# Optimization experiments

Hardware: AMD Instinct MI355X
Metric: run time of the kernel (lower is better)

## Reference

```python
import jax, jax.numpy as jnp
import numpy as np
from jax import lax

BN_EPS = 1e-3  # keras BatchNormalization default epsilon
TOP_K = 2      # keep_top_k


def _conv3(x, k, b, s):
    # x: NDHWC, k: DHWIO, 'SAME' padding like keras Conv3D(padding='same')
    y = lax.conv_general_dilated(x, k, (s, s, s), 'SAME',
                                 dimension_numbers=('NDHWC', 'DHWIO', 'NDHWC'))
    return y + b


def _bn(x, g, be, m, v):
    # inference-mode batch norm with moving statistics
    return g * (x - m) * lax.rsqrt(v + BN_EPS) + be


def setup_inputs() -> dict:
    key = jax.random.key(0)
    ks = jax.random.split(key, 64)
    B, S = 16, 96
    nf, ksz, nE, nb = 32, 3, 8, 4
    inp = {"x": jax.random.normal(ks[0], (B, S, S, S, 1), jnp.float32)}
    cin = 1
    for i in range(nb):
        cout = nf * 2 ** i
        base = 1 + 6 * i
        inp["k%d" % i] = jax.random.normal(ks[base], (ksz, ksz, ksz, cin, cout), jnp.float32) * 0.05
        inp["b%d" % i] = jnp.zeros((cout,), jnp.float32)
        inp["g%d" % i] = 1.0 + 0.1 * jax.random.normal(ks[base + 1], (cout,), jnp.float32)
        inp["be%d" % i] = 0.1 * jax.random.normal(ks[base + 2], (cout,), jnp.float32)
        inp["m%d" % i] = 0.1 * jax.random.normal(ks[base + 3], (cout,), jnp.float32)
        inp["v%d" % i] = jax.random.uniform(ks[base + 4], (cout,), jnp.float32, 0.5, 1.5)
        cin = cout
    c = nf * 2 ** (nb - 1)  # 256
    inp["w1k"] = jax.random.normal(ks[30], (1, 1, 1, c, c), jnp.float32) * 0.05
    inp["w1b"] = jnp.zeros((c,), jnp.float32)
    inp["wg"] = 1.0 + 0.1 * jax.random.normal(ks[31], (c,), jnp.float32)
    inp["wbe"] = 0.1 * jax.random.normal(ks[32], (c,), jnp.float32)
    inp["wm"] = 0.1 * jax.random.normal(ks[33], (c,), jnp.float32)
    inp["wv"] = jax.random.uniform(ks[34], (c,), jnp.float32, 0.5, 1.5)
    inp["w2k"] = jax.random.normal(ks[35], (1, 1, 1, c, nE), jnp.float32) * 0.05
    inp["w2b"] = jnp.zeros((nE,), jnp.float32)
    return inp


def reference(x, k0, b0, g0, be0, m0, v0, k1, b1, g1, be1, m1, v1,
              k2, b2, g2, be2, m2, v2, k3, b3, g3, be3, m3, v3,
              w1k, w1b, wg, wbe, wm, wv, w2k, w2b):
    blocks = [(k0, b0, g0, be0, m0, v0), (k1, b1, g1, be1, m1, v1),
              (k2, b2, g2, be2, m2, v2), (k3, b3, g3, be3, m3, v3)]
    h = x
    for k, b, g, be, m, v in blocks:  # EncoderBlock: Conv3D(stride 2)+BN+ReLU
        h = jax.nn.relu(_bn(_conv3(h, k, b, 2), g, be, m, v))
    h = jnp.mean(h, axis=(1, 2, 3), keepdims=True)  # GAP, [B,1,1,1,256]
    w = _conv3(h, w1k, w1b, 1)
    w = jax.nn.relu(_bn(w, wg, wbe, wm, wv))
    w = _conv3(w, w2k, w2b, 1)  # [B,1,1,1,n_experts]
    # noisy-top-k gating (noise disabled at inference): mask non-top-k to -inf
    top_vals = lax.top_k(w, TOP_K)[0]
    thr = top_vals[..., TOP_K - 1:TOP_K]
    w = jnp.where(w >= thr, w, -jnp.inf)
    return jax.nn.softmax(w, axis=-1)
```

## Files before the change

kernel.cpp:

```cpp
#include <hip/hip_runtime.h>
#include <math.h>

#define BN_EPS 1e-3f

typedef __attribute__((ext_vector_type(8))) unsigned short ushort8v;
typedef __attribute__((ext_vector_type(8))) short short8v;
typedef __attribute__((ext_vector_type(4))) float f32x4;
typedef __attribute__((ext_vector_type(4))) unsigned int uint4v;

__device__ __forceinline__ float4 f4load(const float* p) {
    return *reinterpret_cast<const float4*>(p);
}
__device__ __forceinline__ float bf2f(unsigned short u) {
    union { unsigned int i; float f; } w; w.i = ((unsigned int)u) << 16; return w.f;
}
__device__ __forceinline__ unsigned short f2bf(float f) {
    union { float fv; unsigned int i; } w; w.fv = f;
    unsigned int lsb = (w.i >> 16) & 1u;
    w.i += 0x7fffu + lsb;
    return (unsigned short)(w.i >> 16);
}
__device__ __forceinline__ unsigned cvtpk(float lo, float hi) {
    unsigned r;
    asm("v_cvt_pk_bf16_f32 %0, %1, %2" : "=v"(r) : "v"(lo), "v"(hi));
    return r;
}
__device__ __forceinline__ void st_pair(unsigned short* p0, unsigned short* p1,
                                        float f0, float f1) {
    unsigned u = cvtpk(f0, f1);
    p0[0] = (unsigned short)u;
    p1[0] = (unsigned short)(u >> 16);
}
template<int N> __device__ __forceinline__ void waitv() {
    asm volatile("s_waitcnt vmcnt(%0)" :: "n"(N) : "memory");
}

#define GLOAD_LDS16(g, l)                                                     \
    __builtin_amdgcn_global_load_lds(                                         \
        (const __attribute__((address_space(1))) void*)(const void*)(g),      \
        (__attribute__((address_space(3))) void*)(void*)(l), 16, 0, 0)
#define GLOAD_LDS4(g, l)                                                      \
    __builtin_amdgcn_global_load_lds(                                         \
        (const __attribute__((address_space(1))) void*)(const void*)(g),      \
        (__attribute__((address_space(3))) void*)(void*)(l), 4, 0, 0)

template<int CIN, int COUT>
__device__ __forceinline__ void wprep_body(
    const float* __restrict__ k, unsigned short* __restrict__ wt, int blk)
{
    constexpr int NS = COUT / 16;
    constexpr int KS = CIN / 32;
    int idx = blk * 256 + (int)threadIdx.x;
    if (idx >= 27 * KS * NS * 64) return;
    int lane = idx & 63;
    int nsg  = (idx >> 6) % NS;
    int it   = idx / (64 * NS);
    int tap  = it / KS;
    int ks   = it - tap * KS;
    int sg = lane >> 4, lr = lane & 15;
    int cout = nsg * 16 + lr;
    ushort8v o;
    #pragma unroll
    for (int j = 0; j < 8; ++j) {
        int ci = ks * 32 + sg * 8 + j;
        o[j] = f2bf(k[(size_t)(tap * CIN + ci) * COUT + cout]);
    }
    *reinterpret_cast<ushort8v*>(wt + (size_t)idx * 8) = o;
}

__global__ __launch_bounds__(256) void wprep_all(
    const float* __restrict__ k0,
    const float* __restrict__ k1, const float* __restrict__ k2, const float* __restrict__ k3,
    unsigned short* __restrict__ w0f,
    unsigned short* __restrict__ w1, unsigned short* __restrict__ w2, unsigned short* __restrict__ w3,
    unsigned short* __restrict__ zp)
{
    int b = blockIdx.x;
    if (b < 27)       wprep_body<32, 64>(k1, w1, b);
    else if (b < 135) wprep_body<64, 128>(k2, w2, b - 27);
    else if (b < 567) wprep_body<128, 256>(k3, w3, b - 135);
    else {
        reinterpret_cast<unsigned int*>(zp)[threadIdx.x] = 0u;
        if (threadIdx.x < 128) {
            int ns = threadIdx.x >> 6, lane = threadIdx.x & 63;
            int sg = lane >> 4, lr = lane & 15;
            ushort8v o;
            #pragma unroll
            for (int j = 0; j < 8; ++j) {
                int t = sg * 8 + j;
                o[j] = (t < 27) ? f2bf(k0[t * 32 + ns * 16 + lr]) : (unsigned short)0;
            }
            *reinterpret_cast<ushort8v*>(w0f + (ns * 64 + lane) * 8) = o;
        }
    }
}

__global__ __launch_bounds__(256) void conv0_lds(
    const float* __restrict__ x, const unsigned short* __restrict__ w0f,
    const float* __restrict__ zf,
    const float* __restrict__ b, const float* __restrict__ g,
    const float* __restrict__ be, const float* __restrict__ m,
    const float* __restrict__ v, unsigned short* __restrict__ y)
{
    __shared__ __attribute__((aligned(16))) float tile[81 * 32];
    __shared__ float side[84];
    __shared__ float zslot;

    const int l   = threadIdx.x & 63;
    const int wid = threadIdx.x >> 6;
    const int sg  = l >> 4;
    const int lr  = l & 15;

    int bb = blockIdx.x;
    const int owt = bb % 3;  bb /= 3;
    const int oht = bb % 12; bb /= 12;
    const int odt = bb % 12; const int n = bb / 12;

    const int id0 = odt * 8, ih0 = oht * 8, iw0 = owt * 32;

    if (threadIdx.x == 0) zslot = 0.f;

    #pragma unroll
    for (int q0 = 0; q0 < 648; q0 += 256) {
        int qq = q0 + wid * 64;
        int q = qq + l;
        if (qq < 648 && q < 648) {
            int row = q >> 3, c = q & 7;
            int dd = row / 9, hh = row - dd * 9;
            int id = id0 + dd, ih = ih0 + hh;
            const float* src = (id < 96 && ih < 96)
                ? x + ((size_t)(n * 96 + id) * 96 + ih) * 96 + iw0 + c * 4
                : zf;
            GLOAD_LDS16(src, (char*)tile + (size_t)qq * 16);
        }
    }
    {
        int row = (wid == 0) ? l : ((wid == 1 && l < 17) ? 64 + l : -1);
        if (row >= 0) {
            int dd = row / 9, hh = row - dd * 9;
            int id = id0 + dd, ih = ih0 + hh;
            const float* src = (id < 96 && ih < 96 && iw0 + 32 < 96)
                ? x + ((size_t)(n * 96 + id) * 96 + ih) * 96 + iw0 + 32
                : zf;
            GLOAD_LDS4(src, (char*)side + (wid == 0 ? 0 : 256));
        }
    }
    __syncthreads();

    const short8v B0 = *(const short8v*)(w0f + l * 8);
    const short8v B1 = *(const short8v*)(w0f + (64 + l) * 8);

    int ej[8], wwj[8];
    bool validj[8], sidej[8];
    #pragma unroll
    for (int j = 0; j < 8; ++j) {
        int tap = sg * 8 + j;
        int t = (tap < 27) ? tap : 0;
        int kd = t / 9, r9 = t - kd * 9, kh = r9 / 3, kw = r9 - kh * 3;
        ej[j] = kd * 9 + kh;
        wwj[j] = 2 * lr + kw;
        sidej[j] = (wwj[j] >= 32);
        validj[j] = (tap < 27);
    }

    f32x4 acc[4][2];
    #pragma unroll
    for (int mi = 0; mi < 4; ++mi) {
        acc[mi][0] = (f32x4){0.f, 0.f, 0.f, 0.f};
        acc[mi][1] = (f32x4){0.f, 0.f, 0.f, 0.f};
    }

    #pragma unroll
    for (int mi = 0; mi < 4; ++mi) {
        float av[8];
        #pragma unroll
        for (int j = 0; j < 8; ++j) {
            int row = 18 * wid + 2 * mi + ej[j];
            const float* p = sidej[j] ? &side[row] : &tile[row * 32 + wwj[j]];
            p = validj[j] ? p : &zslot;
            av[j] = *p;
        }
        uint4v au;
        au[0] = cvtpk(av[0], av[1]);
        au[1] = cvtpk(av[2], av[3]);
        au[2] = cvtpk(av[4], av[5]);
        au[3] = cvtpk(av[6], av[7]);
        short8v a = __builtin_bit_cast(short8v, au);
        acc[mi][0] = __builtin_amdgcn_mfma_f32_16x16x32_bf16(a, B0, acc[mi][0], 0, 0, 0);
        acc[mi][1] = __builtin_amdgcn_mfma_f32_16x16x32_bf16(a, B1, acc[mi][1], 0, 0, 0);
    }

    float S[2], T[2];
    #pragma unroll
    for (int ns = 0; ns < 2; ++ns) {
        int c = ns * 16 + lr;
        float sc = g[c] * rsqrtf(v[c] + BN_EPS);
        S[ns] = sc;
        T[ns] = (b[c] - m[c]) * sc + be[c];
    }
    const int odG = odt * 4 + wid;
    #pragma unroll
    for (int mi = 0; mi < 4; ++mi) {
        int oh = oht * 4 + mi;
        unsigned short* yrow =
            y + (((size_t)(n * 48 + odG) * 48 + oh) * 48 + owt * 16) * 32;
        #pragma unroll
        for (int i = 0; i < 4; i += 2) {
            unsigned short* yp0 = yrow + (size_t)(sg * 4 + i) * 32;
            unsigned short* yp1 = yp0 + 32;
            st_pair(yp0 + lr, yp1 + lr,
                    fmaxf(acc[mi][0][i]     * S[0] + T[0], 0.f),
                    fmaxf(acc[mi][0][i + 1] * S[0] + T[0], 0.f));
            st_pair(yp0 + 16 + lr, yp1 + 16 + lr,
                    fmaxf(acc[mi][1][i]     * S[1] + T[1], 0.f),
                    fmaxf(acc[mi][1][i + 1] * S[1] + T[1], 0.f));
        }
    }
}

template<int CIN, int COUT, int INS, int OUTS, int MW, int NSW, int NH,
         int CSPLIT, int KU>
__global__ __launch_bounds__(256, 2) void conv_mfma_lds(
    const unsigned short* __restrict__ x, const unsigned short* __restrict__ wt,
    const unsigned short* __restrict__ zp,
    const float* __restrict__ b, const float* __restrict__ g,
    const float* __restrict__ be, const float* __restrict__ m,
    const float* __restrict__ v, unsigned short* __restrict__ y)
{
    constexpr int NSfull = COUT / 16;
    constexpr int NSB = NSW * NH;
    constexpr int KS = CIN / 32;
    constexpr int NITK = 27 * KS;
    constexpr int NIT = NITK / KU;
    constexpr int MGROUPS = 4 / NH;
    constexpr int MTILE = MGROUPS * MW * 16;
    constexpr int BSTEP = NSB * KU * 1024;
    constexpr int ASTEP = MGROUPS * MW * KU * 1024;
    constexpr int STRIDE = BSTEP + ASTEP;
    constexpr int BL = (NSB * KU) / 4;
    constexpr int AL = MW * KU;
    static_assert(NSB * CSPLIT == NSfull && NITK % KU == 0 && (NSB * KU) % 4 == 0, "tiling");
    static_assert(NIT >= 3, "pipeline depth");

    __shared__ __attribute__((aligned(16))) char lds[3 * STRIDE];

    const int l   = threadIdx.x & 63;
    const int wid = threadIdx.x >> 6;
    const int sg  = l >> 4;
    const int lr  = l & 15;

    const int mblk   = blockIdx.x / CSPLIT;
    const int cchunk = blockIdx.x % CSPLIT;
    const int mgroup = wid / NH;
    const int ngroup = wid % NH;
    const int gCoutBase = (cchunk * NSB + ngroup * NSW) * 16;
    const int vwave = mblk * MTILE + mgroup * MW * 16;

    const unsigned short* ap0[MW];
    unsigned smask[MW];
    #pragma unroll
    for (int mi = 0; mi < MW; ++mi) {
        int vA = vwave + mi * 16 + lr;
        int owA = vA % OUTS; int t1 = vA / OUTS;
        int ohA = t1 % OUTS; int t2 = t1 / OUTS;
        int odA = t2 % OUTS; int nA = t2 / OUTS;
        ap0[mi] = x + ((((size_t)nA * INS + 2 * odA) * INS + 2 * ohA) * INS + 2 * owA) * CIN + sg * 8;
        smask[mi] = ((odA == OUTS - 1) ? 0x07FC0000u : 0u)
                  | ((ohA == OUTS - 1) ? 0x070381C0u : 0u)
                  | ((owA == OUTS - 1) ? 0x04924924u : 0u);
    }

    const unsigned short* zpl = (const unsigned short*)((const char*)zp + l * 16);

    f32x4 acc[MW][NSW];
    #pragma unroll
    for (int mi = 0; mi < MW; ++mi)
        #pragma unroll
        for (int ns = 0; ns < NSW; ++ns) acc[mi][ns] = (f32x4){0.f, 0.f, 0.f, 0.f};

    auto stage = [&](int ito, int p) {
        char* dst = &lds[p * STRIDE];
        #pragma unroll
        for (int c = 0; c < BL; ++c) {
            int idx  = c * 256 + (int)threadIdx.x;
            int lane = idx & 63;
            int sub  = idx >> 6;
            int u    = sub / NSB;
            int grp  = sub % NSB;
            int it   = ito * KU + u;
            const unsigned short* src =
                wt + ((size_t)(it * NSfull + cchunk * NSB + grp) * 64 + lane) * 8;
            GLOAD_LDS16(src, dst + sub * 1024);
        }
        if (ngroup == 0) {
            #pragma unroll
            for (int u = 0; u < KU; ++u) {
                int it = ito * KU + u;
                int tap = (KS == 1) ? it : it / KS;
                int ks  = (KS == 1) ? 0  : it - tap * KS;
                int kd = tap / 9, r9 = tap - kd * 9, kh = r9 / 3, kw = r9 - kh * 3;
                size_t aoff = (size_t)((kd * INS + kh) * INS + kw) * CIN + ks * 32;
                #pragma unroll
                for (int mi = 0; mi < MW; ++mi) {
                    const unsigned short* ga =
                        ((smask[mi] >> tap) & 1u) ? zpl : (ap0[mi] + aoff);
                    GLOAD_LDS16(ga, dst + BSTEP + ((mgroup * MW + mi) * KU + u) * 1024);
                }
            }
        }
    };

    auto computestep = [&](const char* buf) {
        #pragma unroll
        for (int u = 0; u < KU; ++u) {
            short8v Bf[NSW], Af[MW];
            #pragma unroll
            for (int ns = 0; ns < NSW; ++ns)
                Bf[ns] = *(const short8v*)(buf + (u * NSB + ngroup * NSW + ns) * 1024 + l * 16);
            #pragma unroll
            for (int mi = 0; mi < MW; ++mi)
                Af[mi] = *(const short8v*)(buf + BSTEP + ((mgroup * MW + mi) * KU + u) * 1024 + l * 16);
            #pragma unroll
            for (int mi = 0; mi < MW; ++mi)
                #pragma unroll
                for (int ns = 0; ns < NSW; ++ns)
                    acc[mi][ns] = __builtin_amdgcn_mfma_f32_16x16x32_bf16(Af[mi], Bf[ns], acc[mi][ns], 0, 0, 0);
        }
    };

    stage(0, 0);
    stage(1, 1);
    #pragma unroll 1
    for (int ito = 0; ito < NIT - 1; ++ito) {
        if (ngroup == 0) waitv<BL + AL>(); else waitv<BL>();
        __builtin_amdgcn_s_barrier();
        asm volatile("" ::: "memory");
        if (ito + 2 < NIT) stage(ito + 2, (ito + 2) % 3);
        computestep(&lds[(ito % 3) * STRIDE]);
    }
    waitv<0>();
    __builtin_amdgcn_s_barrier();
    asm volatile("" ::: "memory");
    computestep(&lds[((NIT - 1) % 3) * STRIDE]);

    float S[NSW], T[NSW];
    #pragma unroll
    for (int ns = 0; ns < NSW; ++ns) {
        int c = gCoutBase + ns * 16 + lr;
        float sc = g[c] * rsqrtf(v[c] + BN_EPS);
        S[ns] = sc;
        T[ns] = (b[c] - m[c]) * sc + be[c];
    }
    #pragma unroll
    for (int mi = 0; mi < MW; ++mi) {
        #pragma unroll
        for (int i = 0; i < 4; i += 2) {
            int vD0 = vwave + mi * 16 + sg * 4 + i;
            int vD1 = vD0 + 1;
            int ow0 = vD0 % OUTS; int u1 = vD0 / OUTS;
            int oh0 = u1 % OUTS; int u2 = u1 / OUTS;
            int od0 = u2 % OUTS; int n0 = u2 / OUTS;
            unsigned short* yp0 =
                y + ((((size_t)n0 * OUTS + od0) * OUTS + oh0) * OUTS + ow0) * COUT + gCoutBase + lr;
            int ow1 = vD1 % OUTS; int w1 = vD1 / OUTS;
            int oh1 = w1 % OUTS; int w2 = w1 / OUTS;
            int od1 = w2 % OUTS; int n1 = w2 / OUTS;
            unsigned short* yp1 =
                y + ((((size_t)n1 * OUTS + od1) * OUTS + oh1) * OUTS + ow1) * COUT + gCoutBase + lr;
            #pragma unroll
            for (int ns = 0; ns < NSW; ++ns)
                st_pair(yp0 + ns * 16, yp1 + ns * 16,
                        fmaxf(acc[mi][ns][i]     * S[ns] + T[ns], 0.f),
                        fmaxf(acc[mi][ns][i + 1] * S[ns] + T[ns], 0.f));
        }
    }
}

__global__ __launch_bounds__(256) void head_kernel(
    const unsigned short* __restrict__ x4,
    const float* __restrict__ w1k, const float* __restrict__ w1b,
    const float* __restrict__ wg,  const float* __restrict__ wbe,
    const float* __restrict__ wm,  const float* __restrict__ wv,
    const float* __restrict__ w2k, const float* __restrict__ w2b,
    float* __restrict__ out)
{
    __shared__ float part[8][256];
    __shared__ float h[256];
    __shared__ float r[256];
    __shared__ float logits[8];

    const int n = blockIdx.x;
    const int t = threadIdx.x;
    const int c8 = t & 31;
    const int pg = t >> 5;

    const unsigned short* xb = x4 + (size_t)n * 216 * 256 + c8 * 8;
    float s[8] = {0.f, 0.f, 0.f, 0.f, 0.f, 0.f, 0.f, 0.f};
    for (int i = pg; i < 216; i += 8) {
        ushort8v v8 = *reinterpret_cast<const ushort8v*>(xb + (size_t)i * 256);
        #pragma unroll
        for (int j = 0; j < 8; ++j) s[j] += bf2f(v8[j]);
    }
    #pragma unroll
    for (int j = 0; j < 8; ++j) part[pg][c8 * 8 + j] = s[j];
    __syncthreads();

    float a = 0.f;
    #pragma unroll
    for (int gi = 0; gi < 8; ++gi) a += part[gi][t];
    h[t] = a * (1.0f / 216.0f);
    __syncthreads();

    float acc = w1b[t];
    #pragma unroll 4
    for (int ci = 0; ci < 256; ++ci) acc += h[ci] * w1k[ci * 256 + t];
    float sc = wg[t] * rsqrtf(wv[t] + BN_EPS);
    acc = (acc - wm[t]) * sc + wbe[t];
    r[t] = fmaxf(acc, 0.f);
    __syncthreads();

    if (t < 8) {
        float a2 = w2b[t];
        for (int ci = 0; ci < 256; ++ci) a2 += r[ci] * w2k[ci * 8 + t];
        logits[t] = a2;
    }
    __syncthreads();

    if (t == 0) {
        float m1 = -INFINITY, m2 = -INFINITY;
        for (int e = 0; e < 8; ++e) {
            float val = logits[e];
            if (val > m1) { m2 = m1; m1 = val; }
            else if (val > m2) { m2 = val; }
        }
        float thr = m2;
        float ex[8]; float sum = 0.f;
        for (int e = 0; e < 8; ++e) {
            float val = (logits[e] >= thr) ? logits[e] : -INFINITY;
            ex[e] = expf(val - m1);
            sum += ex[e];
        }
        float inv = 1.0f / sum;
        for (int e = 0; e < 8; ++e) out[n * 8 + e] = ex[e] * inv;
    }
}

extern "C" void kernel_launch(void* const* d_in, const int* in_sizes, int n_in,
                              void* d_out, int out_size, void* d_ws, size_t ws_size,
                              hipStream_t stream) {
    const float* x   = (const float*)d_in[0];
    const float* k0  = (const float*)d_in[1];
    const float* b0  = (const float*)d_in[2];
    const float* g0  = (const float*)d_in[3];
    const float* be0 = (const float*)d_in[4];
    const float* m0  = (const float*)d_in[5];
    const float* v0  = (const float*)d_in[6];
    const float* k1  = (const float*)d_in[7];
    const float* b1  = (const float*)d_in[8];
    const float* g1  = (const float*)d_in[9];
    const float* be1 = (const float*)d_in[10];
    const float* m1  = (const float*)d_in[11];
    const float* v1  = (const float*)d_in[12];
    const float* k2  = (const float*)d_in[13];
    const float* b2  = (const float*)d_in[14];
    const float* g2  = (const float*)d_in[15];
    const float* be2 = (const float*)d_in[16];
    const float* m2  = (const float*)d_in[17];
    const float* v2  = (const float*)d_in[18];
    const float* k3  = (const float*)d_in[19];
    const float* b3  = (const float*)d_in[20];
    const float* g3  = (const float*)d_in[21];
    const float* be3 = (const float*)d_in[22];
    const float* m3  = (const float*)d_in[23];
    const float* v3  = (const float*)d_in[24];
    const float* w1k = (const float*)d_in[25];
    const float* w1b = (const float*)d_in[26];
    const float* wg  = (const float*)d_in[27];
    const float* wbe = (const float*)d_in[28];
    const float* wm  = (const float*)d_in[29];
    const float* wv  = (const float*)d_in[30];
    const float* w2k = (const float*)d_in[31];
    const float* w2b = (const float*)d_in[32];

    unsigned short* x1  = (unsigned short*)d_ws;
    unsigned short* x2  = x1 + 56623104;
    unsigned short* x3  = x2 + 14155776;
    unsigned short* x4  = x3 + 3538944;
    unsigned short* Wt1 = x4 + 884736;
    unsigned short* Wt2 = Wt1 + 55296;
    unsigned short* Wt3 = Wt2 + 221184;
    unsigned short* zp  = Wt3 + 884736;
    unsigned short* W0f = zp + 512;

    wprep_all<<<568, 256, 0, stream>>>(k0, k1, k2, k3, W0f, Wt1, Wt2, Wt3, zp);
    conv0_lds<<<6912, 256, 0, stream>>>(x, W0f, (const float*)zp, b0, g0, be0, m0, v0, x1);
    conv_mfma_lds<32, 64, 48, 24, 2, 4, 1, 1, 1><<<1728, 256, 0, stream>>>(x1, Wt1, zp, b1, g1, be1, m1, v1, x2);
    conv_mfma_lds<64, 128, 24, 12, 1, 4, 2, 1, 1><<<864, 256, 0, stream>>>(x2, Wt2, zp, b2, g2, be2, m2, v2, x3);
    conv_mfma_lds<128, 256, 12, 6, 1, 1, 4, 4, 2><<<864, 256, 0, stream>>>(x3, Wt3, zp, b3, g3, be3, m3, v3, x4);
    head_kernel<<<16, 256, 0, stream>>>(x4, w1k, w1b, wg, wbe, wm, wv, w2k, w2b, (float*)d_out);
}
```

Baseline: 195.8 us.

## Restructure conv0 tap layout with padded LDS tile and register-cached rows

```diff
diff --git a/kernel.cpp b/kernel.cpp
--- a/kernel.cpp
+++ b/kernel.cpp
@@ -39,10 +39,6 @@
     __builtin_amdgcn_global_load_lds(                                         \
         (const __attribute__((address_space(1))) void*)(const void*)(g),      \
         (__attribute__((address_space(3))) void*)(void*)(l), 16, 0, 0)
-#define GLOAD_LDS4(g, l)                                                      \
-    __builtin_amdgcn_global_load_lds(                                         \
-        (const __attribute__((address_space(1))) void*)(const void*)(g),      \
-        (__attribute__((address_space(3))) void*)(void*)(l), 4, 0, 0)
 
 template<int CIN, int COUT>
 __device__ __forceinline__ void wprep_body(
@@ -81,16 +77,21 @@
     else if (b < 567) wprep_body<128, 256>(k3, w3, b - 135);
     else {
         reinterpret_cast<unsigned int*>(zp)[threadIdx.x] = 0u;
-        if (threadIdx.x < 128) {
-            int ns = threadIdx.x >> 6, lane = threadIdx.x & 63;
+        {
+            int t = (int)threadIdx.x;
+            int lane = t & 63;
+            int mf = (t >> 6) & 1;
+            int ns = t >> 7;
             int sg = lane >> 4, lr = lane & 15;
             ushort8v o;
             #pragma unroll
             for (int j = 0; j < 8; ++j) {
-                int t = sg * 8 + j;
-                o[j] = (t < 27) ? f2bf(k0[t * 32 + ns * 16 + lr]) : (unsigned short)0;
+                int jj = mf * 8 + j;
+                bool valid = (sg < 3) && (jj < 9);
+                int tap = sg * 9 + jj;
+                o[j] = valid ? f2bf(k0[tap * 32 + ns * 16 + lr]) : (unsigned short)0;
             }
-            *reinterpret_cast<ushort8v*>(w0f + (ns * 64 + lane) * 8) = o;
+            *reinterpret_cast<ushort8v*>(w0f + (size_t)t * 8) = o;
         }
     }
 }
@@ -102,9 +103,7 @@
     const float* __restrict__ be, const float* __restrict__ m,
     const float* __restrict__ v, unsigned short* __restrict__ y)
 {
-    __shared__ __attribute__((aligned(16))) float tile[81 * 32];
-    __shared__ float side[84];
-    __shared__ float zslot;
+    __shared__ __attribute__((aligned(16))) float tile[81 * 36];
 
     const int l   = threadIdx.x & 63;
     const int wid = threadIdx.x >> 6;
@@ -118,49 +117,38 @@
 
     const int id0 = odt * 8, ih0 = oht * 8, iw0 = owt * 32;
 
-    if (threadIdx.x == 0) zslot = 0.f;
-
-    #pragma unroll
-    for (int q0 = 0; q0 < 648; q0 += 256) {
+    #pragma unroll
+    for (int q0 = 0; q0 < 729; q0 += 256) {
         int qq = q0 + wid * 64;
-        int q = qq + l;
-        if (qq < 648 && q < 648) {
-            int row = q >> 3, c = q & 7;
+        int q  = qq + l;
+        if (qq < 729 && q < 729) {
+            int row = q / 9, c = q - row * 9;
             int dd = row / 9, hh = row - dd * 9;
             int id = id0 + dd, ih = ih0 + hh;
-            const float* src = (id < 96 && ih < 96)
+            const float* src =
+                (id < 96 && ih < 96 && (c < 8 || iw0 + 32 < 96))
                 ? x + ((size_t)(n * 96 + id) * 96 + ih) * 96 + iw0 + c * 4
                 : zf;
             GLOAD_LDS16(src, (char*)tile + (size_t)qq * 16);
         }
     }
+    __syncthreads();
+
+    const short8v B00 = *(const short8v*)(w0f + (size_t)(0 * 64 + l) * 8);
+    const short8v B01 = *(const short8v*)(w0f + (size_t)(1 * 64 + l) * 8);
+    const short8v B10 = *(const short8v*)(w0f + (size_t)(2 * 64 + l) * 8);
+    const short8v B11 = *(const short8v*)(w0f + (size_t)(3 * 64 + l) * 8);
+
+    float rc[9][3];
     {
-        int row = (wid == 0) ? l : ((wid == 1 && l < 17) ? 64 + l : -1);
-        if (row >= 0) {
-            int dd = row / 9, hh = row - dd * 9;
-            int id = id0 + dd, ih = ih0 + hh;
-            const float* src = (id < 96 && ih < 96 && iw0 + 32 < 96)
-                ? x + ((size_t)(n * 96 + id) * 96 + ih) * 96 + iw0 + 32
-                : zf;
-            GLOAD_LDS4(src, (char*)side + (wid == 0 ? 0 : 256));
-        }
-    }
-    __syncthreads();
-
-    const short8v B0 = *(const short8v*)(w0f + l * 8);
-    const short8v B1 = *(const short8v*)(w0f + (64 + l) * 8);
-
-    int ej[8], wwj[8];
-    bool validj[8], sidej[8];
-    #pragma unroll
-    for (int j = 0; j < 8; ++j) {
-        int tap = sg * 8 + j;
-        int t = (tap < 27) ? tap : 0;
-        int kd = t / 9, r9 = t - kd * 9, kh = r9 / 3, kw = r9 - kh * 3;
-        ej[j] = kd * 9 + kh;
-        wwj[j] = 2 * lr + kw;
-        sidej[j] = (wwj[j] >= 32);
-        validj[j] = (tap < 27);
+        int dcl = (sg < 3) ? (2 * wid + sg) : 0;
+        const float* rb = tile + (size_t)(dcl * 9) * 36 + 2 * lr;
+        #pragma unroll
+        for (int r = 0; r < 9; ++r) {
+            float2 lo = *reinterpret_cast<const float2*>(rb + r * 36);
+            rc[r][0] = lo.x; rc[r][1] = lo.y;
+            rc[r][2] = rb[r * 36 + 2];
+        }
     }
 
     f32x4 acc[4][2];
@@ -172,22 +160,21 @@
 
     #pragma unroll
     for (int mi = 0; mi < 4; ++mi) {
-        float av[8];
-        #pragma unroll
-        for (int j = 0; j < 8; ++j) {
-            int row = 18 * wid + 2 * mi + ej[j];
-            const float* p = sidej[j] ? &side[row] : &tile[row * 32 + wwj[j]];
-            p = validj[j] ? p : &zslot;
-            av[j] = *p;
-        }
-        uint4v au;
-        au[0] = cvtpk(av[0], av[1]);
-        au[1] = cvtpk(av[2], av[3]);
-        au[2] = cvtpk(av[4], av[5]);
-        au[3] = cvtpk(av[6], av[7]);
-        short8v a = __builtin_bit_cast(short8v, au);
-        acc[mi][0] = __builtin_amdgcn_mfma_f32_16x16x32_bf16(a, B0, acc[mi][0], 0, 0, 0);
-        acc[mi][1] = __builtin_amdgcn_mfma_f32_16x16x32_bf16(a, B1, acc[mi][1], 0, 0, 0);
+        const int h0 = 2 * mi;
+        uint4v au0;
+        au0[0] = cvtpk(rc[h0][0],     rc[h0][1]);
+        au0[1] = cvtpk(rc[h0][2],     rc[h0 + 1][0]);
+        au0[2] = cvtpk(rc[h0 + 1][1], rc[h0 + 1][2]);
+        au0[3] = cvtpk(rc[h0 + 2][0], rc[h0 + 2][1]);
+        short8v a0 = __builtin_bit_cast(short8v, au0);
+        uint4v au1;
+        au1[0] = cvtpk(rc[h0 + 2][2], 0.f);
+        au1[1] = 0; au1[2] = 0; au1[3] = 0;
+        short8v a1 = __builtin_bit_cast(short8v, au1);
+        acc[mi][0] = __builtin_amdgcn_mfma_f32_16x16x32_bf16(a0, B00, acc[mi][0], 0, 0, 0);
+        acc[mi][0] = __builtin_amdgcn_mfma_f32_16x16x32_bf16(a1, B01, acc[mi][0], 0, 0, 0);
+        acc[mi][1] = __builtin_amdgcn_mfma_f32_16x16x32_bf16(a0, B10, acc[mi][1], 0, 0, 0);
+        acc[mi][1] = __builtin_amdgcn_mfma_f32_16x16x32_bf16(a1, B11, acc[mi][1], 0, 0, 0);
     }
 
     float S[2], T[2];
@@ -494,7 +481,7 @@
 
     wprep_all<<<568, 256, 0, stream>>>(k0, k1, k2, k3, W0f, Wt1, Wt2, Wt3, zp);
     conv0_lds<<<6912, 256, 0, stream>>>(x, W0f, (const float*)zp, b0, g0, be0, m0, v0, x1);
-    conv_mfma_lds<32, 64, 48, 24, 2, 4, 1, 1, 1><<<1728, 256, 0, stream>>>(x1, Wt1, zp, b1, g1, be1, m1, v1, x2);
+    conv_mfma_lds<32, 64, 48, 24, 3, 4, 1, 1, 1><<<1152, 256, 0, stream>>>(x1, Wt1, zp, b1, g1, be1, m1, v1, x2);
     conv_mfma_lds<64, 128, 24, 12, 1, 4, 2, 1, 1><<<864, 256, 0, stream>>>(x2, Wt2, zp, b2, g2, be2, m2, v2, x3);
     conv_mfma_lds<128, 256, 12, 6, 1, 1, 4, 4, 2><<<864, 256, 0, stream>>>(x3, Wt3, zp, b3, g3, be3, m3, v3, x4);
     head_kernel<<<16, 256, 0, stream>>>(x4, w1k, w1b, wg, wbe, wm, wv, w2k, w2b, (float*)d_out);
```

After: 196.4 us. No clear change (+0.3%).
